# Optimization experiments

Measured on AMD Instinct MI355X. Metric: run time of the kernel, lower is better.

The kernel has to match this reference:

```python
import jax, jax.numpy as jnp
import numpy as np

B, H, L, D = 4, 8, 2048, 64
FACTOR = 5


def setup_inputs() -> dict:
    key = jax.random.key(0)
    kq, kk, kv, ki = jax.random.split(key, 4)
    sample_k = min(FACTOR * int(np.ceil(np.log(L))), L)  # = 40
    queries = jax.random.normal(kq, (B, H, L, D), jnp.float32)
    keys = jax.random.normal(kk, (B, H, L, D), jnp.float32)
    values = jax.random.normal(kv, (B, H, L, D), jnp.float32)
    index_sample = jax.random.randint(ki, (L, sample_k), 0, L)
    return {"queries": queries, "keys": keys, "values": values,
            "index_sample": index_sample}


def prob_attention(queries, keys, values, index_sample):
    Bq, Hq, L_Q, Dk = queries.shape
    L_K = keys.shape[2]
    n_top = min(FACTOR * int(np.ceil(np.log(L_Q))), L_Q)  # u
    scale = float(1.0 / np.sqrt(Dk))

    # --- _prob_QK: sample scores for each query over random key subset ---
    # K_sample: (B,H,L_Q,S,D); index_sample shared across batch/heads
    K_sample = keys[:, :, index_sample, :]
    Q_K_sample = jnp.einsum('bhld,bhlsd->bhls', queries, K_sample)
    # sparsity measure M = max - mean (mean over full L_K as in source)
    M = Q_K_sample.max(-1) - Q_K_sample.sum(-1) / L_K      # (B,H,L_Q)
    M_top = jax.lax.top_k(M, n_top)[1]                     # (B,H,u) query indices

    # full scores only for the selected "active" queries
    Q_reduce = jnp.take_along_axis(queries, M_top[..., None], axis=2)  # (B,H,u,D)
    scores = jnp.einsum('bhud,bhkd->bhuk', Q_reduce, keys) * scale     # (B,H,u,L_K)

    # --- causal ProbMask: key j masked when j > selected query position ---
    causal = jnp.arange(L_K)[None, None, None, :] > M_top[..., None]
    scores = jnp.where(causal, -jnp.inf, scores)
    attn = jax.nn.softmax(scores, axis=-1)
    ctx_update = jnp.einsum('bhuk,bhkd->bhud', attn, values)           # (B,H,u,D)

    # --- initial context (causal branch): running cumulative sum of V ---
    context = jnp.cumsum(values, axis=2)                               # (B,H,L_Q,D)

    # scatter active-query results back into the context
    b_idx = jnp.arange(Bq)[:, None, None]
    h_idx = jnp.arange(Hq)[None, :, None]
    context = context.at[b_idx, h_idx, M_top].set(ctx_update)
    return context


def reference(queries, keys, values, index_sample):
    return prob_attention(queries, keys, values, index_sample)
```

## Files before the change

### kernel.cpp

```cpp
#include <hip/hip_runtime.h>
#include <hip/hip_bf16.h>
#include <cstdint>

#define BB 4
#define HH 8
#define LL 2048
#define DD 64
#define SK 40
#define NT 40
#define BHN (BB*HH)
#define SCALE 0.125f
#define CHUNK 128
#define NCH (LL/CHUNK)
#define USPL 5
#define UPB (NT/USPL)

#define WS_M    0
#define WS_SUB  (WS_M + BHN*LL)
#define WS_CTX  (WS_SUB + BHN*64*DD)
#define WS_PM   (WS_CTX + BHN*NT*DD)
#define WS_PSUM (WS_PM + BHN*NT*NCH)
#define WS_PACC (WS_PSUM + BHN*NT*NCH)
#define WS_TOP  (WS_PACC + BHN*NT*NCH*DD)

static __device__ __forceinline__ float4 f4add(float4 a, float4 b) {
    float4 r; r.x = a.x + b.x; r.y = a.y + b.y; r.z = a.z + b.z; r.w = a.w + b.w; return r;
}

__global__ __launch_bounds__(256) void k1_M(const float* __restrict__ Q,
                                            const float* __restrict__ K,
                                            const int* __restrict__ isamp,
                                            float* __restrict__ M) {
    int bid  = blockIdx.x;
    int swz  = (bid & 7) * (BHN * LL / 4 / 8) + (bid >> 3);
    int wid  = swz * 4 + (threadIdx.x >> 6);
    int lane = threadIdx.x & 63;
    int bh   = wid >> 11;
    int l    = wid & (LL - 1);
    int g    = lane >> 4;
    int e    = lane & 15;

    float4 q = reinterpret_cast<const float4*>(Q + (size_t)wid * DD)[e];
    const float* Kbh = K + (size_t)bh * LL * DD;
    const int* irow = isamp + l * SK;

    int idxs[SK / 4];
#pragma unroll
    for (int p = 0; p < SK / 4; p++) idxs[p] = irow[p * 4 + g];

    float mx = -INFINITY, sm = 0.f;
#pragma unroll
    for (int b = 0; b < 2; b++) {
        float4 kv[5];
#pragma unroll
        for (int i = 0; i < 5; i++)
            kv[i] = reinterpret_cast<const float4*>(Kbh + (size_t)idxs[b * 5 + i] * DD)[e];
        float dd[5];
#pragma unroll
        for (int i = 0; i < 5; i++)
            dd[i] = q.x * kv[i].x + q.y * kv[i].y + q.z * kv[i].z + q.w * kv[i].w;
#pragma unroll
        for (int i = 0; i < 5; i++) {
            float d = dd[i];
            d += __shfl_xor(d, 1);
            d += __shfl_xor(d, 2);
            d += __shfl_xor(d, 4);
            d += __shfl_xor(d, 8);
            mx = fmaxf(mx, d);
            sm += d;
        }
    }
    mx = fmaxf(mx, __shfl_xor(mx, 16));
    mx = fmaxf(mx, __shfl_xor(mx, 32));
    sm += __shfl_xor(sm, 16);
    sm += __shfl_xor(sm, 32);
    if (lane == 0) M[wid] = mx - sm * (1.0f / (float)LL);
}

__global__ __launch_bounds__(64) void k2_topk(const float* __restrict__ M,
                                              int* __restrict__ Mtop) {
    int bh = blockIdx.x, lane = threadIdx.x;
    const float* Mb = M + (size_t)bh * LL;
    unsigned long long key[32];
#pragma unroll
    for (int j = 0; j < 32; j++) {
        int i = lane + j * 64;
        unsigned u = __float_as_uint(Mb[i]);
        u = (u & 0x80000000u) ? ~u : (u | 0x80000000u);
        key[j] = ((unsigned long long)u << 32) | (unsigned)(~i);
    }
    unsigned long long winner = 0ull;
    for (int t = 0; t < NT; t++) {
        unsigned long long best = 0ull;
#pragma unroll
        for (int j = 0; j < 32; j++) {
            unsigned long long k = key[j];
            k = (k == winner) ? 0ull : k;
            key[j] = k;
            best = (k > best) ? k : best;
        }
#pragma unroll
        for (int off = 32; off; off >>= 1) {
            unsigned long long o = __shfl_xor(best, off);
            best = (o > best) ? o : best;
        }
        winner = best;
        if (lane == 0) Mtop[bh * NT + t] = (int)(~(unsigned)(best & 0xFFFFFFFFull));
    }
}

__global__ __launch_bounds__(256) void k3a_partial(const float* __restrict__ Q,
                                                   const float* __restrict__ K,
                                                   const float* __restrict__ V,
                                                   const int* __restrict__ Mtop,
                                                   float* __restrict__ pm,
                                                   float* __restrict__ psum,
                                                   float* __restrict__ pacc) {
    __shared__ float q_lds[UPB * DD];
    __shared__ float s_lds[UPB][CHUNK];
    __shared__ int   qi_lds[UPB];
    int bid = blockIdx.x;
    int swz = (bid & 7) * (BHN * NCH * USPL / 8) + (bid >> 3);
    int bh  = swz / (NCH * USPL);
    int rem = swz % (NCH * USPL);
    int ch  = rem / USPL;
    int u0  = (rem % USPL) * UPB;
    int ck  = ch * CHUNK;
    int tid = threadIdx.x;

    if (tid < UPB) qi_lds[tid] = Mtop[bh * NT + u0 + tid];
    __syncthreads();
    for (int c = tid; c < UPB * 16; c += 256) {
        int u = c >> 4, j = c & 15;
        reinterpret_cast<float4*>(q_lds)[c] =
            reinterpret_cast<const float4*>(Q + ((size_t)bh * LL + qi_lds[u]) * DD)[j];
    }
    __syncthreads();

    int k    = ck + (tid >> 1);
    int half = tid & 1;
    const float4* krow = reinterpret_cast<const float4*>(K + ((size_t)bh * LL + k) * DD) + half * 8;
    float4 kreg[8];
#pragma unroll
    for (int j = 0; j < 8; j++) kreg[j] = krow[j];
#pragma unroll
    for (int u = 0; u < UPB; u++) {
        const float4* q4 = reinterpret_cast<const float4*>(q_lds + u * DD) + half * 8;
        float d = 0.f;
#pragma unroll
        for (int j = 0; j < 8; j++) {
            float4 a = q4[j], b = kreg[j];
            d += a.x * b.x + a.y * b.y + a.z * b.z + a.w * b.w;
        }
        d += __shfl_xor(d, 1);
        float s = (k <= qi_lds[u]) ? d * SCALE : -INFINITY;
        if (half == 0) s_lds[u][k - ck] = s;
    }
    __syncthreads();

    int w = tid >> 6, lane = tid & 63;
#pragma unroll
    for (int uu = 0; uu < UPB / 4; uu++) {
        int u = w + uu * 4;
        float s0 = s_lds[u][lane], s1 = s_lds[u][lane + 64];
        float m = fmaxf(s0, s1);
#pragma unroll
        for (int off = 32; off; off >>= 1) m = fmaxf(m, __shfl_xor(m, off));
        float e0 = (s0 == -INFINITY) ? 0.f : __expf(s0 - m);
        float e1 = (s1 == -INFINITY) ? 0.f : __expf(s1 - m);
        s_lds[u][lane] = e0;
        s_lds[u][lane + 64] = e1;
        float smv = e0 + e1;
#pragma unroll
        for (int off = 32; off; off >>= 1) smv += __shfl_xor(smv, off);
        if (lane == 0) {
            size_t rg = (size_t)bh * NT + u0 + u;
            pm  [rg * NCH + ch] = m;
            psum[rg * NCH + ch] = smv;
        }
    }
    __syncthreads();

    float acc[UPB / 4] = {};
    const float* vbase = V + ((size_t)bh * LL + ck) * DD + lane;
#pragma unroll 4
    for (int kk = 0; kk < CHUNK; kk++) {
        float v = vbase[(size_t)kk * DD];
#pragma unroll
        for (int uu = 0; uu < UPB / 4; uu++)
            acc[uu] += s_lds[w + uu * 4][kk] * v;
    }
#pragma unroll
    for (int uu = 0; uu < UPB / 4; uu++) {
        size_t rg = (size_t)bh * NT + u0 + w + uu * 4;
        pacc[(rg * NCH + ch) * DD + lane] = acc[uu];
    }
}

__global__ __launch_bounds__(256) void k4a_sub(const float* __restrict__ V,
                                               float* __restrict__ sub) {
    __shared__ float4 part[16][16];
    int blk = blockIdx.x;
    int t = threadIdx.x;
    int d4 = t & 15, rg = t >> 4;
    const float4* v4 = reinterpret_cast<const float4*>(V) + (size_t)blk * 32 * 16 + (size_t)rg * 2 * 16 + d4;
    float4 a = v4[0], b = v4[16];
    part[rg][d4] = f4add(a, b);
    __syncthreads();
#pragma unroll
    for (int step = 8; step; step >>= 1) {
        if (rg < step) part[rg][d4] = f4add(part[rg][d4], part[rg + step][d4]);
        __syncthreads();
    }
    if (rg == 0)
        reinterpret_cast<float4*>(sub)[(size_t)blk * 16 + d4] = part[0][d4];
}

__global__ __launch_bounds__(256) void k4b_scan(const float* __restrict__ V,
                                                const float* __restrict__ sub,
                                                const float* __restrict__ pm,
                                                const float* __restrict__ psum,
                                                const float* __restrict__ pacc,
                                                const int* __restrict__ Mtop,
                                                float* __restrict__ out) {
    __shared__ float4 plds[16][16];
    int blk = blockIdx.x;
    int bh = blk >> 6, j = blk & 63;
    int t = threadIdx.x;
    int d4 = t & 15, rg = t >> 4;

    const float4* sub4 = reinterpret_cast<const float4*>(sub) + (size_t)(bh * 64) * 16 + d4;
    float4 off = {0.f, 0.f, 0.f, 0.f};
    for (int p = 0; p < j; p++) off = f4add(off, sub4[(size_t)p * 16]);

    const float4* v4 = reinterpret_cast<const float4*>(V) + (size_t)blk * 32 * 16 + (size_t)rg * 2 * 16 + d4;
    float4 a = v4[0], b = v4[16];
    plds[rg][d4] = f4add(a, b);
    __syncthreads();
    float4 ex = {0.f, 0.f, 0.f, 0.f};
    for (int p = 0; p < rg; p++) ex = f4add(ex, plds[p][d4]);

    float4 r0 = f4add(f4add(off, ex), a);
    float4 r1 = f4add(r0, b);
    float4* o4 = reinterpret_cast<float4*>(out) + (size_t)blk * 32 * 16 + (size_t)rg * 2 * 16 + d4;
    o4[0] = r0;
    o4[16] = r1;
    __syncthreads();

    if (t < DD) {
        for (int u = 0; u < NT; u++) {
            int qi = Mtop[bh * NT + u];
            if ((qi >> 5) != j) continue;
            size_t row = (size_t)bh * NT + u;
            float pmv[NCH];
            float m = -INFINITY;
#pragma unroll
            for (int i = 0; i < NCH; i++) {
                pmv[i] = pm[row * NCH + i];
                m = fmaxf(m, pmv[i]);
            }
            float Z = 0.f, acc = 0.f;
#pragma unroll
            for (int i = 0; i < NCH; i++) {
                float sc = (pmv[i] == -INFINITY) ? 0.f : __expf(pmv[i] - m);
                Z   += psum[row * NCH + i] * sc;
                acc += pacc[(row * NCH + i) * DD + t] * sc;
            }
            out[((size_t)bh * LL + qi) * DD + t] = acc / Z;
        }
    }
}

extern "C" void kernel_launch(void* const* d_in, const int* in_sizes, int n_in,
                              void* d_out, int out_size, void* d_ws, size_t ws_size,
                              hipStream_t stream) {
    const float* Q = (const float*)d_in[0];
    const float* K = (const float*)d_in[1];
    const float* V = (const float*)d_in[2];
    const int* isamp = (const int*)d_in[3];
    float* ws   = (float*)d_ws;
    float* M    = ws + WS_M;
    float* sub  = ws + WS_SUB;
    float* pm   = ws + WS_PM;
    float* psum = ws + WS_PSUM;
    float* pacc = ws + WS_PACC;
    int*   Mtop = (int*)(ws + WS_TOP);
    float* out  = (float*)d_out;

    k1_M       <<<BHN * LL / 4,      256, 0, stream>>>(Q, K, isamp, M);
    k2_topk    <<<BHN,                64, 0, stream>>>(M, Mtop);
    k3a_partial<<<BHN * NCH * USPL,  256, 0, stream>>>(Q, K, V, Mtop, pm, psum, pacc);
    k4a_sub    <<<BHN * 64,          256, 0, stream>>>(V, sub);
    k4b_scan   <<<BHN * 64,          256, 0, stream>>>(V, sub, pm, psum, pacc, Mtop, out);
}
```

Measured before the change: 213.0 us.

## Fuse independent kernels, reorder scan before attention, vectorize PV accumulation

Merges the sampled-score kernel with the V block-sum kernel, and the top-k kernel with the cumulative-sum scan, as heterogeneous blocks in one launch each. This cuts five launches to four and lets the independent work run side by side. The active-query merge moves into a small scatter kernel that runs after the scan, so the scan no longer loops over all 40 rows per block. The partial attention kernel uses 20 queries per block instead of 8 and float4 V loads with a cross-lane reduction. The trade-off is fewer blocks in that kernel and the top-k branch idling 192 of its 256 threads.

```diff
diff --git a/kernel.cpp b/kernel.cpp
--- a/kernel.cpp
+++ b/kernel.cpp
@@ -12,7 +12,7 @@
 #define SCALE 0.125f
 #define CHUNK 128
 #define NCH (LL/CHUNK)
-#define USPL 5
+#define USPL 2
 #define UPB (NT/USPL)
 
 #define WS_M    0
@@ -23,89 +23,144 @@
 #define WS_PACC (WS_PSUM + BHN*NT*NCH)
 #define WS_TOP  (WS_PACC + BHN*NT*NCH*DD)
 
+#define K1_BLOCKS (BHN * LL / 4)
+#define K4A_BLOCKS (BHN * 64)
+#define K4B_BLOCKS (BHN * 64)
+
 static __device__ __forceinline__ float4 f4add(float4 a, float4 b) {
     float4 r; r.x = a.x + b.x; r.y = a.y + b.y; r.z = a.z + b.z; r.w = a.w + b.w; return r;
 }
 
-__global__ __launch_bounds__(256) void k1_M(const float* __restrict__ Q,
-                                            const float* __restrict__ K,
-                                            const int* __restrict__ isamp,
-                                            float* __restrict__ M) {
-    int bid  = blockIdx.x;
-    int swz  = (bid & 7) * (BHN * LL / 4 / 8) + (bid >> 3);
-    int wid  = swz * 4 + (threadIdx.x >> 6);
-    int lane = threadIdx.x & 63;
-    int bh   = wid >> 11;
-    int l    = wid & (LL - 1);
-    int g    = lane >> 4;
-    int e    = lane & 15;
-
-    float4 q = reinterpret_cast<const float4*>(Q + (size_t)wid * DD)[e];
-    const float* Kbh = K + (size_t)bh * LL * DD;
-    const int* irow = isamp + l * SK;
-
-    int idxs[SK / 4];
-#pragma unroll
-    for (int p = 0; p < SK / 4; p++) idxs[p] = irow[p * 4 + g];
-
-    float mx = -INFINITY, sm = 0.f;
-#pragma unroll
-    for (int b = 0; b < 2; b++) {
-        float4 kv[5];
-#pragma unroll
-        for (int i = 0; i < 5; i++)
-            kv[i] = reinterpret_cast<const float4*>(Kbh + (size_t)idxs[b * 5 + i] * DD)[e];
-        float dd[5];
-#pragma unroll
-        for (int i = 0; i < 5; i++)
-            dd[i] = q.x * kv[i].x + q.y * kv[i].y + q.z * kv[i].z + q.w * kv[i].w;
-#pragma unroll
-        for (int i = 0; i < 5; i++) {
-            float d = dd[i];
-            d += __shfl_xor(d, 1);
-            d += __shfl_xor(d, 2);
-            d += __shfl_xor(d, 4);
-            d += __shfl_xor(d, 8);
-            mx = fmaxf(mx, d);
-            sm += d;
-        }
-    }
-    mx = fmaxf(mx, __shfl_xor(mx, 16));
-    mx = fmaxf(mx, __shfl_xor(mx, 32));
-    sm += __shfl_xor(sm, 16);
-    sm += __shfl_xor(sm, 32);
-    if (lane == 0) M[wid] = mx - sm * (1.0f / (float)LL);
-}
-
-__global__ __launch_bounds__(64) void k2_topk(const float* __restrict__ M,
-                                              int* __restrict__ Mtop) {
-    int bh = blockIdx.x, lane = threadIdx.x;
-    const float* Mb = M + (size_t)bh * LL;
-    unsigned long long key[32];
-#pragma unroll
-    for (int j = 0; j < 32; j++) {
-        int i = lane + j * 64;
-        unsigned u = __float_as_uint(Mb[i]);
-        u = (u & 0x80000000u) ? ~u : (u | 0x80000000u);
-        key[j] = ((unsigned long long)u << 32) | (unsigned)(~i);
-    }
-    unsigned long long winner = 0ull;
-    for (int t = 0; t < NT; t++) {
-        unsigned long long best = 0ull;
+__global__ __launch_bounds__(256) void f1_m_sub(const float* __restrict__ Q,
+                                                const float* __restrict__ K,
+                                                const int* __restrict__ isamp,
+                                                const float* __restrict__ V,
+                                                float* __restrict__ M,
+                                                float* __restrict__ sub) {
+    int bid = blockIdx.x;
+    if (bid < K1_BLOCKS) {
+        int swz  = (bid & 7) * (K1_BLOCKS / 8) + (bid >> 3);
+        int wid  = swz * 4 + (threadIdx.x >> 6);
+        int lane = threadIdx.x & 63;
+        int bh   = wid >> 11;
+        int l    = wid & (LL - 1);
+        int g    = lane >> 4;
+        int e    = lane & 15;
+
+        float4 q = reinterpret_cast<const float4*>(Q + (size_t)wid * DD)[e];
+        const float* Kbh = K + (size_t)bh * LL * DD;
+        const int* irow = isamp + l * SK;
+
+        int idxs[SK / 4];
+#pragma unroll
+        for (int p = 0; p < SK / 4; p++) idxs[p] = irow[p * 4 + g];
+
+        float mx = -INFINITY, sm = 0.f;
+#pragma unroll
+        for (int b = 0; b < 2; b++) {
+            float4 kv[5];
+#pragma unroll
+            for (int i = 0; i < 5; i++)
+                kv[i] = reinterpret_cast<const float4*>(Kbh + (size_t)idxs[b * 5 + i] * DD)[e];
+            float dd[5];
+#pragma unroll
+            for (int i = 0; i < 5; i++)
+                dd[i] = q.x * kv[i].x + q.y * kv[i].y + q.z * kv[i].z + q.w * kv[i].w;
+#pragma unroll
+            for (int i = 0; i < 5; i++) {
+                float d = dd[i];
+                d += __shfl_xor(d, 1);
+                d += __shfl_xor(d, 2);
+                d += __shfl_xor(d, 4);
+                d += __shfl_xor(d, 8);
+                mx = fmaxf(mx, d);
+                sm += d;
+            }
+        }
+        mx = fmaxf(mx, __shfl_xor(mx, 16));
+        mx = fmaxf(mx, __shfl_xor(mx, 32));
+        sm += __shfl_xor(sm, 16);
+        sm += __shfl_xor(sm, 32);
+        if (lane == 0) M[wid] = mx - sm * (1.0f / (float)LL);
+    } else {
+        __shared__ float4 part[16][16];
+        int blk = bid - K1_BLOCKS;
+        int t = threadIdx.x;
+        int d4 = t & 15, rg = t >> 4;
+        const float4* v4 = reinterpret_cast<const float4*>(V) + (size_t)blk * 32 * 16 + (size_t)rg * 2 * 16 + d4;
+        float4 a = v4[0], b = v4[16];
+        part[rg][d4] = f4add(a, b);
+        __syncthreads();
+#pragma unroll
+        for (int step = 8; step; step >>= 1) {
+            if (rg < step) part[rg][d4] = f4add(part[rg][d4], part[rg + step][d4]);
+            __syncthreads();
+        }
+        if (rg == 0)
+            reinterpret_cast<float4*>(sub)[(size_t)blk * 16 + d4] = part[0][d4];
+    }
+}
+
+__global__ __launch_bounds__(256) void f2_topk_scan(const float* __restrict__ M,
+                                                    int* __restrict__ Mtop,
+                                                    const float* __restrict__ V,
+                                                    const float* __restrict__ sub,
+                                                    float* __restrict__ out) {
+    int bid = blockIdx.x;
+    if (bid < BHN) {
+        int lane = threadIdx.x;
+        if (lane >= 64) return;
+        int bh = bid;
+        const float* Mb = M + (size_t)bh * LL;
+        unsigned long long key[32];
 #pragma unroll
         for (int j = 0; j < 32; j++) {
-            unsigned long long k = key[j];
-            k = (k == winner) ? 0ull : k;
-            key[j] = k;
-            best = (k > best) ? k : best;
-        }
-#pragma unroll
-        for (int off = 32; off; off >>= 1) {
-            unsigned long long o = __shfl_xor(best, off);
-            best = (o > best) ? o : best;
-        }
-        winner = best;
-        if (lane == 0) Mtop[bh * NT + t] = (int)(~(unsigned)(best & 0xFFFFFFFFull));
+            int i = lane + j * 64;
+            unsigned u = __float_as_uint(Mb[i]);
+            u = (u & 0x80000000u) ? ~u : (u | 0x80000000u);
+            key[j] = ((unsigned long long)u << 32) | (unsigned)(~i);
+        }
+        unsigned long long winner = 0ull;
+        for (int t = 0; t < NT; t++) {
+            unsigned long long best = 0ull;
+#pragma unroll
+            for (int j = 0; j < 32; j++) {
+                unsigned long long k = key[j];
+                k = (k == winner) ? 0ull : k;
+                key[j] = k;
+                best = (k > best) ? k : best;
+            }
+#pragma unroll
+            for (int off = 32; off; off >>= 1) {
+                unsigned long long o = __shfl_xor(best, off);
+                best = (o > best) ? o : best;
+            }
+            winner = best;
+            if (lane == 0) Mtop[bh * NT + t] = (int)(~(unsigned)(best & 0xFFFFFFFFull));
+        }
+    } else {
+        __shared__ float4 plds[16][16];
+        int blk = bid - BHN;
+        int bh = blk >> 6, j = blk & 63;
+        int t = threadIdx.x;
+        int d4 = t & 15, rg = t >> 4;
+
+        const float4* sub4 = reinterpret_cast<const float4*>(sub) + (size_t)(bh * 64) * 16 + d4;
+        float4 off = {0.f, 0.f, 0.f, 0.f};
+        for (int p = 0; p < j; p++) off = f4add(off, sub4[(size_t)p * 16]);
+
+        const float4* v4 = reinterpret_cast<const float4*>(V) + (size_t)blk * 32 * 16 + (size_t)rg * 2 * 16 + d4;
+        float4 a = v4[0], b = v4[16];
+        plds[rg][d4] = f4add(a, b);
+        __syncthreads();
+        float4 ex = {0.f, 0.f, 0.f, 0.f};
+        for (int p = 0; p < rg; p++) ex = f4add(ex, plds[p][d4]);
+
+        float4 r0 = f4add(f4add(off, ex), a);
+        float4 r1 = f4add(r0, b);
+        float4* o4 = reinterpret_cast<float4*>(out) + (size_t)blk * 32 * 16 + (size_t)rg * 2 * 16 + d4;
+        o4[0] = r0;
+        o4[16] = r1;
     }
 }
 
@@ -121,10 +176,10 @@
     __shared__ int   qi_lds[UPB];
     int bid = blockIdx.x;
     int swz = (bid & 7) * (BHN * NCH * USPL / 8) + (bid >> 3);
-    int bh  = swz / (NCH * USPL);
-    int rem = swz % (NCH * USPL);
-    int ch  = rem / USPL;
-    int u0  = (rem % USPL) * UPB;
+    int bh  = swz >> 5;
+    int rem = swz & 31;
+    int ch  = rem >> 1;
+    int u0  = (rem & 1) * UPB;
     int ck  = ch * CHUNK;
     int tid = threadIdx.x;
 
@@ -143,7 +198,7 @@
     float4 kreg[8];
 #pragma unroll
     for (int j = 0; j < 8; j++) kreg[j] = krow[j];
-#pragma unroll
+#pragma unroll 4
     for (int u = 0; u < UPB; u++) {
         const float4* q4 = reinterpret_cast<const float4*>(q_lds + u * DD) + half * 8;
         float d = 0.f;
@@ -181,94 +236,62 @@
     }
     __syncthreads();
 
-    float acc[UPB / 4] = {};
-    const float* vbase = V + ((size_t)bh * LL + ck) * DD + lane;
+    int d4 = lane & 15, kp = lane >> 4;
+    float4 acc[UPB / 4];
+#pragma unroll
+    for (int uu = 0; uu < UPB / 4; uu++) acc[uu] = make_float4(0.f, 0.f, 0.f, 0.f);
+    const float4* v4 = reinterpret_cast<const float4*>(V + ((size_t)bh * LL + ck) * DD) + d4;
 #pragma unroll 4
-    for (int kk = 0; kk < CHUNK; kk++) {
-        float v = vbase[(size_t)kk * DD];
-#pragma unroll
-        for (int uu = 0; uu < UPB / 4; uu++)
-            acc[uu] += s_lds[w + uu * 4][kk] * v;
+    for (int kb = 0; kb < CHUNK; kb += 4) {
+        int kk = kb + kp;
+        float4 v = v4[(size_t)kk * 16];
+#pragma unroll
+        for (int uu = 0; uu < UPB / 4; uu++) {
+            float s = s_lds[w + uu * 4][kk];
+            acc[uu].x += s * v.x;
+            acc[uu].y += s * v.y;
+            acc[uu].z += s * v.z;
+            acc[uu].w += s * v.w;
+        }
     }
 #pragma unroll
     for (int uu = 0; uu < UPB / 4; uu++) {
-        size_t rg = (size_t)bh * NT + u0 + w + uu * 4;
-        pacc[(rg * NCH + ch) * DD + lane] = acc[uu];
-    }
-}
-
-__global__ __launch_bounds__(256) void k4a_sub(const float* __restrict__ V,
-                                               float* __restrict__ sub) {
-    __shared__ float4 part[16][16];
-    int blk = blockIdx.x;
-    int t = threadIdx.x;
-    int d4 = t & 15, rg = t >> 4;
-    const float4* v4 = reinterpret_cast<const float4*>(V) + (size_t)blk * 32 * 16 + (size_t)rg * 2 * 16 + d4;
-    float4 a = v4[0], b = v4[16];
-    part[rg][d4] = f4add(a, b);
-    __syncthreads();
-#pragma unroll
-    for (int step = 8; step; step >>= 1) {
-        if (rg < step) part[rg][d4] = f4add(part[rg][d4], part[rg + step][d4]);
-        __syncthreads();
-    }
-    if (rg == 0)
-        reinterpret_cast<float4*>(sub)[(size_t)blk * 16 + d4] = part[0][d4];
-}
-
-__global__ __launch_bounds__(256) void k4b_scan(const float* __restrict__ V,
-                                                const float* __restrict__ sub,
-                                                const float* __restrict__ pm,
-                                                const float* __restrict__ psum,
-                                                const float* __restrict__ pacc,
-                                                const int* __restrict__ Mtop,
-                                                float* __restrict__ out) {
-    __shared__ float4 plds[16][16];
-    int blk = blockIdx.x;
-    int bh = blk >> 6, j = blk & 63;
-    int t = threadIdx.x;
-    int d4 = t & 15, rg = t >> 4;
-
-    const float4* sub4 = reinterpret_cast<const float4*>(sub) + (size_t)(bh * 64) * 16 + d4;
-    float4 off = {0.f, 0.f, 0.f, 0.f};
-    for (int p = 0; p < j; p++) off = f4add(off, sub4[(size_t)p * 16]);
-
-    const float4* v4 = reinterpret_cast<const float4*>(V) + (size_t)blk * 32 * 16 + (size_t)rg * 2 * 16 + d4;
-    float4 a = v4[0], b = v4[16];
-    plds[rg][d4] = f4add(a, b);
-    __syncthreads();
-    float4 ex = {0.f, 0.f, 0.f, 0.f};
-    for (int p = 0; p < rg; p++) ex = f4add(ex, plds[p][d4]);
-
-    float4 r0 = f4add(f4add(off, ex), a);
-    float4 r1 = f4add(r0, b);
-    float4* o4 = reinterpret_cast<float4*>(out) + (size_t)blk * 32 * 16 + (size_t)rg * 2 * 16 + d4;
-    o4[0] = r0;
-    o4[16] = r1;
-    __syncthreads();
-
-    if (t < DD) {
-        for (int u = 0; u < NT; u++) {
-            int qi = Mtop[bh * NT + u];
-            if ((qi >> 5) != j) continue;
-            size_t row = (size_t)bh * NT + u;
-            float pmv[NCH];
-            float m = -INFINITY;
-#pragma unroll
-            for (int i = 0; i < NCH; i++) {
-                pmv[i] = pm[row * NCH + i];
-                m = fmaxf(m, pmv[i]);
-            }
-            float Z = 0.f, acc = 0.f;
-#pragma unroll
-            for (int i = 0; i < NCH; i++) {
-                float sc = (pmv[i] == -INFINITY) ? 0.f : __expf(pmv[i] - m);
-                Z   += psum[row * NCH + i] * sc;
-                acc += pacc[(row * NCH + i) * DD + t] * sc;
-            }
-            out[((size_t)bh * LL + qi) * DD + t] = acc / Z;
-        }
-    }
+        float4 a = acc[uu];
+        a.x += __shfl_xor(a.x, 16); a.x += __shfl_xor(a.x, 32);
+        a.y += __shfl_xor(a.y, 16); a.y += __shfl_xor(a.y, 32);
+        a.z += __shfl_xor(a.z, 16); a.z += __shfl_xor(a.z, 32);
+        a.w += __shfl_xor(a.w, 16); a.w += __shfl_xor(a.w, 32);
+        if (kp == 0) {
+            size_t rg = (size_t)bh * NT + u0 + w + uu * 4;
+            reinterpret_cast<float4*>(pacc + (rg * NCH + ch) * DD)[d4] = a;
+        }
+    }
+}
+
+__global__ __launch_bounds__(64) void k3b_scatter(const float* __restrict__ pm,
+                                                  const float* __restrict__ psum,
+                                                  const float* __restrict__ pacc,
+                                                  const int* __restrict__ Mtop,
+                                                  float* __restrict__ out) {
+    int row = blockIdx.x;
+    int lane = threadIdx.x;
+    int bh = row / NT;
+    float pmv[NCH];
+    float m = -INFINITY;
+#pragma unroll
+    for (int i = 0; i < NCH; i++) {
+        pmv[i] = pm[(size_t)row * NCH + i];
+        m = fmaxf(m, pmv[i]);
+    }
+    float Z = 0.f, acc = 0.f;
+#pragma unroll
+    for (int i = 0; i < NCH; i++) {
+        float sc = (pmv[i] == -INFINITY) ? 0.f : __expf(pmv[i] - m);
+        Z   += psum[(size_t)row * NCH + i] * sc;
+        acc += pacc[((size_t)row * NCH + i) * DD + lane] * sc;
+    }
+    int qi = Mtop[row];
+    out[((size_t)bh * LL + qi) * DD + lane] = acc / Z;
 }
 
 extern "C" void kernel_launch(void* const* d_in, const int* in_sizes, int n_in,
@@ -287,9 +310,8 @@
     int*   Mtop = (int*)(ws + WS_TOP);
     float* out  = (float*)d_out;
 
-    k1_M       <<<BHN * LL / 4,      256, 0, stream>>>(Q, K, isamp, M);
-    k2_topk    <<<BHN,                64, 0, stream>>>(M, Mtop);
-    k3a_partial<<<BHN * NCH * USPL,  256, 0, stream>>>(Q, K, V, Mtop, pm, psum, pacc);
-    k4a_sub    <<<BHN * 64,          256, 0, stream>>>(V, sub);
-    k4b_scan   <<<BHN * 64,          256, 0, stream>>>(V, sub, pm, psum, pacc, Mtop, out);
-}
+    f1_m_sub    <<<K1_BLOCKS + K4A_BLOCKS, 256, 0, stream>>>(Q, K, isamp, V, M, sub);
+    f2_topk_scan<<<BHN + K4B_BLOCKS,       256, 0, stream>>>(M, Mtop, V, sub, out);
+    k3a_partial <<<BHN * NCH * USPL,       256, 0, stream>>>(Q, K, V, Mtop, pm, psum, pacc);
+    k3b_scatter <<<BHN * NT,                64, 0, stream>>>(pm, psum, pacc, Mtop, out);
+}
```

Result: faster. 176.9 us (-16.9%).
